# Kernel tuning notes

Measured on AMD Instinct MI355X. Metric: run time of the kernel, lower is better.

Reference implementation:

```python
import jax, jax.numpy as jnp
import numpy as np

SAMPLE_RATE = 44100
MAX_DURATION = 5.0
IR_LEN = int(SAMPLE_RATE * MAX_DURATION)   # 220500 taps (~5 s reverb tail)
AUDIO_LEN = SAMPLE_RATE * 60               # 60 s of mono audio


def setup_inputs() -> dict:
    key = jax.random.key(0)
    k1, k2 = jax.random.split(key)
    audio = jax.random.normal(k1, (1, AUDIO_LEN), dtype=jnp.float32)
    ir = jax.random.normal(k2, (IR_LEN,), dtype=jnp.float32)  # learned impulse response parameter
    return {"audio": audio, "ir": ir}


def _fft_correlate_valid(audio, ir):
    """Valid cross-correlation of (audio zero-padded by M-1) with ir.

    Matches torch: pad audio with M-1 trailing zeros, then conv1d (which is
    cross-correlation) in 'valid' mode -> output length N. Computed via FFT
    (O(N log N)) instead of direct O(N*M) convolution; identical math up to
    floating-point rounding.
    """
    B, N = audio.shape
    M = ir.shape[0]
    full = (N + M - 1) + M - 1          # full linear conv length of padded signal
    nfft = 1 << int(np.ceil(np.log2(full)))
    # trailing zero-pad covers both the explicit M-1 padding and FFT padding
    x = jnp.pad(audio, ((0, 0), (0, nfft - N)))
    k = jnp.pad(ir[::-1], (0, nfft - M))  # flip kernel: conv(x, flip(ir)) == correlate(x, ir)
    y = jnp.fft.irfft(jnp.fft.rfft(x, axis=-1) * jnp.fft.rfft(k), n=nfft, axis=-1)
    # valid cross-correlation region of the padded signal: indices [M-1, M-1+N)
    return jax.lax.dynamic_slice_in_dim(y, M - 1, N, axis=-1)


def reference(audio, ir):
    y = _fft_correlate_valid(audio, ir)       # [1, N]
    return y / jnp.max(jnp.abs(y))            # global max-abs normalization
```

## Files before the change

kernel.cpp:

```cpp
#include <hip/hip_runtime.h>
#include <hip/hip_fp16.h>


#define L_FFT (1 << 20)
#define GSTRIDE 273
#define PSCALE (1.0f / 1048576.0f)

__device__ __forceinline__ float2 h2f(__half2 h) { return __half22float2(h); }
__device__ __forceinline__ __half2 f2h(float2 v) { return __floats2half2_rn(v.x, v.y); }

__device__ __forceinline__ float2 cmul(float2 a, float2 b) {
    return make_float2(a.x * b.x - a.y * b.y, a.x * b.y + a.y * b.x);
}

__device__ __forceinline__ void rad4(float2 a, float2 b, float2 c, float2 d,
                                     float2& o0, float2& o1, float2& o2, float2& o3) {
    float2 apc = make_float2(a.x + c.x, a.y + c.y);
    float2 amc = make_float2(a.x - c.x, a.y - c.y);
    float2 bpd = make_float2(b.x + d.x, b.y + d.y);
    float2 bmd = make_float2(b.x - d.x, b.y - d.y);
    o0 = make_float2(apc.x + bpd.x, apc.y + bpd.y);
    o2 = make_float2(apc.x - bpd.x, apc.y - bpd.y);
    o1 = make_float2(amc.x + bmd.y, amc.y - bmd.x);
    o3 = make_float2(amc.x - bmd.y, amc.y + bmd.x);
}

__device__ __forceinline__ void dft16(float2 x[16]) {
    float2 tt[16];
    rad4(x[0], x[4], x[8],  x[12], tt[0],  tt[1],  tt[2],  tt[3]);
    rad4(x[1], x[5], x[9],  x[13], tt[4],  tt[5],  tt[6],  tt[7]);
    rad4(x[2], x[6], x[10], x[14], tt[8],  tt[9],  tt[10], tt[11]);
    rad4(x[3], x[7], x[11], x[15], tt[12], tt[13], tt[14], tt[15]);
    const float C1 = 0.92387953251128675613f, S1 = 0.38268343236508977173f;
    const float C2 = 0.70710678118654752440f;
    const float2 W1 = make_float2( C1, -S1);
    const float2 W2 = make_float2( C2, -C2);
    const float2 W3 = make_float2( S1, -C1);
    const float2 W6 = make_float2(-C2, -C2);
    const float2 W9 = make_float2(-C1,  S1);
    tt[5]  = cmul(tt[5],  W1);
    tt[6]  = cmul(tt[6],  W2);
    tt[7]  = cmul(tt[7],  W3);
    tt[9]  = cmul(tt[9],  W2);
    tt[10] = make_float2(tt[10].y, -tt[10].x);
    tt[11] = cmul(tt[11], W6);
    tt[13] = cmul(tt[13], W3);
    tt[14] = cmul(tt[14], W6);
    tt[15] = cmul(tt[15], W9);
    rad4(tt[0], tt[4], tt[8],  tt[12], x[0], x[4], x[8],  x[12]);
    rad4(tt[1], tt[5], tt[9],  tt[13], x[1], x[5], x[9],  x[13]);
    rad4(tt[2], tt[6], tt[10], tt[14], x[2], x[6], x[10], x[14]);
    rad4(tt[3], tt[7], tt[11], tt[15], x[3], x[7], x[11], x[15]);
}

__device__ __forceinline__ void fft256_core(float2 x[16], int i, int gi,
                                            float2* lds) {
    dft16(x);
    float sa, ca;
    __sincosf(-6.28318530717958647692f * (float)i * (1.0f / 256.0f), &sa, &ca);
    float2 w1 = make_float2(ca, sa);
    float2 w = w1;
#pragma unroll
    for (int k1 = 1; k1 < 16; ++k1) {
        x[k1] = cmul(x[k1], w);
        w = cmul(w, w1);
    }
    float2* base = lds + gi * GSTRIDE;
#pragma unroll
    for (int k1 = 0; k1 < 16; ++k1) base[i * 17 + k1] = x[k1];
    __syncthreads();
#pragma unroll
    for (int q1 = 0; q1 < 16; ++q1) x[q1] = base[q1 * 17 + i];
    dft16(x);
}

__device__ __forceinline__ void stage256_store(float2 x[16], __half2* db,
                                               int g, int i, int J, int log2J,
                                               float invLn) {
    int j = g & (J - 1);
    int np = g >> log2J;
    float base = -6.28318530717958647692f * (float)np * invLn;
    float sa, ca;
    __sincosf(base * (float)i, &sa, &ca);
    float2 w = make_float2(ca, sa);
    __sincosf(base * 16.0f, &sa, &ca);
    float2 w16 = make_float2(ca, sa);
    size_t ob = (size_t)256 * (g - j) + j;
#pragma unroll
    for (int k2 = 0; k2 < 16; ++k2) {
        db[ob + (size_t)(i + 16 * k2) * J] = f2h(cmul(x[k2], w));
        w = cmul(w, w16);
    }
}

__device__ __forceinline__ void store_j1_coalesced(float2 x[16], __half2* db,
                                                   int bx, int gi, int i, int tid,
                                                   float2* lds, float invL) {
    int g = bx * 16 + gi;
    float base = -6.28318530717958647692f * (float)g * invL;
    float sa, ca;
    __sincosf(base * (float)i, &sa, &ca);
    float2 w = make_float2(ca, sa);
    __sincosf(base * 16.0f, &sa, &ca);
    float2 w16 = make_float2(ca, sa);
    __syncthreads();
#pragma unroll
    for (int k2 = 0; k2 < 16; ++k2) {
        int e = 256 * gi + i + 16 * k2;
        lds[e + (e >> 8)] = cmul(x[k2], w);
        w = cmul(w, w16);
    }
    __syncthreads();
    __half2* dwin = db + (size_t)4096 * bx;
#pragma unroll
    for (int c = 0; c < 16; ++c) {
        int e2 = tid + 256 * c;
        dwin[e2] = f2h(lds[e2 + (e2 >> 8)]);
    }
}

__global__ void fwd1_pack(const float* __restrict__ audio,
                          const float* __restrict__ ir,
                          __half2* __restrict__ dst, int N, int M, int V) {
    __shared__ float2 lds[16 * GSTRIDE];
    int tid = threadIdx.x;
    int gi = tid & 15, i = tid >> 4;
    int bx = blockIdx.x, slot = blockIdx.y;
    int g = bx * 16 + gi;
    __half2* db = dst + (size_t)slot * L_FFT;

    float2 x[16];
#pragma unroll
    for (int q2 = 0; q2 < 16; ++q2) {
        int idx = g + (i + 16 * q2) * (L_FFT / 256);
        float2 v;
        if (slot == 0) {
            v = make_float2(audio[idx], audio[idx + V]);
        } else if (slot == 1) {
            float a2 = (idx + 2 * V < N) ? audio[idx + 2 * V] : 0.f;
            float a3 = (idx + 3 * V < N) ? audio[idx + 3 * V] : 0.f;
            v = make_float2(a2, a3);
        } else {
            v = make_float2((idx < M) ? ir[idx] : 0.f, 0.f);
        }
        x[q2] = v;
    }
    fft256_core(x, i, gi, lds);
    store_j1_coalesced(x, db, bx, gi, i, tid, lds, 1.0f / (float)L_FFT);
}

__global__ void stage256(const __half2* __restrict__ src, __half2* __restrict__ dst,
                         int J, int log2J, float invLn) {
    __shared__ float2 lds[16 * GSTRIDE];
    int tid = threadIdx.x;
    int gi = tid & 15, i = tid >> 4;
    int g = blockIdx.x * 16 + gi;
    size_t boff = (size_t)blockIdx.y * L_FFT;
    const __half2* sb = src + boff;
    __half2* db = dst + boff;
    float2 x[16];
#pragma unroll
    for (int q2 = 0; q2 < 16; ++q2)
        x[q2] = h2f(sb[g + (i + 16 * q2) * (L_FFT / 256)]);
    fft256_core(x, i, gi, lds);
    stage256_store(x, db, g, i, J, log2J, invLn);
}

__global__ void mid_spectral_inv1(const __half2* __restrict__ A,
                                  __half2* __restrict__ B) {
    __shared__ float2 lds[16 * GSTRIDE];
    int tid = threadIdx.x;
    int gi = tid & 15, i = tid >> 4;
    int bx = blockIdx.x;
    size_t boff = (size_t)blockIdx.y * L_FFT;
    int g = bx * 16 + gi;
    int gmid = g + (i << 12);

    const __half2* sa = A + boff;
    const __half2* sh = A + (size_t)2 * L_FFT;
    float2 x[16], h[16];
#pragma unroll
    for (int q = 0; q < 16; ++q) {
        x[q] = h2f(sa[gmid + (size_t)q * 65536]);
        h[q] = h2f(sh[gmid + (size_t)q * 65536]);
    }
    dft16(x);
    dft16(h);
#pragma unroll
    for (int r = 0; r < 16; ++r) {
        float2 Z = x[r], H = h[r];
        x[r] = make_float2((Z.x * H.x + Z.y * H.y) * PSCALE,
                           (Z.x * H.y - Z.y * H.x) * PSCALE);
    }
    fft256_core(x, i, gi, lds);
    store_j1_coalesced(x, B + boff, bx, gi, i, tid, lds, 1.0f / (float)L_FFT);
}

__global__ void inv3_max(const __half2* __restrict__ src,
                         float* __restrict__ partials, int N, int V) {
    int g = blockIdx.x * blockDim.x + threadIdx.x;
    int p = blockIdx.y;
    const __half2* sb = src + (size_t)p * L_FFT;
    float2 x[16];
#pragma unroll
    for (int q = 0; q < 16; ++q) x[q] = h2f(sb[g + q * 65536]);
    dft16(x);
    int lenO = (p == 1) ? (N - 3 * V) : V;
    float m = 0.f;
#pragma unroll
    for (int r = 0; r < 16; ++r) {
        int n = g + r * 65536;
        if (n < V)    m = fmaxf(m, fabsf(x[r].x));
        if (n < lenO) m = fmaxf(m, fabsf(x[r].y));
    }
    for (int o = 32; o > 0; o >>= 1) m = fmaxf(m, __shfl_xor(m, o));
    __shared__ float sm[4];
    int lane = threadIdx.x & 63, wv = threadIdx.x >> 6;
    if (lane == 0) sm[wv] = m;
    __syncthreads();
    if (threadIdx.x == 0)
        partials[blockIdx.y * gridDim.x + blockIdx.x] =
            fmaxf(fmaxf(sm[0], sm[1]), fmaxf(sm[2], sm[3]));
}

__global__ void norm_final(const __half2* __restrict__ src,
                           float* __restrict__ out,
                           const float* __restrict__ partials, int N, int V) {
    __shared__ float sm[4];
    int tid = threadIdx.x;
    int g = blockIdx.x * blockDim.x + tid;
    int p = blockIdx.y;
    const __half2* sb = src + (size_t)p * L_FFT;
    float2 x[16];
#pragma unroll
    for (int q = 0; q < 16; ++q) x[q] = h2f(sb[g + q * 65536]);

    float m = 0.f;
    for (int i = tid; i < 512; i += 256) m = fmaxf(m, partials[i]);
    for (int o = 32; o > 0; o >>= 1) m = fmaxf(m, __shfl_xor(m, o));
    int lane = tid & 63, wv = tid >> 6;
    if (lane == 0) sm[wv] = m;
    __syncthreads();
    float inv = 1.0f / fmaxf(fmaxf(sm[0], sm[1]), fmaxf(sm[2], sm[3]));

    dft16(x);
    int se = 2 * p, so = 2 * p + 1;
    int lenO = (p == 1) ? (N - 3 * V) : V;
#pragma unroll
    for (int r = 0; r < 16; ++r) {
        int n = g + r * 65536;
        if (n < V)    out[(size_t)se * V + n] = x[r].x * inv;
        if (n < lenO) out[(size_t)so * V + n] = -x[r].y * inv;
    }
}

extern "C" void kernel_launch(void* const* d_in, const int* in_sizes, int n_in,
                              void* d_out, int out_size, void* d_ws, size_t ws_size,
                              hipStream_t stream) {
    const float* audio = (const float*)d_in[0];
    const float* ir    = (const float*)d_in[1];
    float* out = (float*)d_out;

    const int N = in_sizes[0];
    const int M = in_sizes[1];
    const int V = L_FFT - M + 1;

    __half2* A = (__half2*)d_ws;
    __half2* B = A + (size_t)3 * L_FFT;
    float* partials = (float*)(B + (size_t)3 * L_FFT);

    const float invLn2 = 1.0f / 4096.0f;

    fwd1_pack<<<dim3(256, 3), 256, 0, stream>>>(audio, ir, B, N, M, V);
    stage256<<<dim3(256, 3), 256, 0, stream>>>(B, A, 256, 8, invLn2);
    mid_spectral_inv1<<<dim3(256, 2), 256, 0, stream>>>(A, B);
    stage256<<<dim3(256, 2), 256, 0, stream>>>(B, A, 256, 8, invLn2);
    inv3_max<<<dim3(256, 2), 256, 0, stream>>>(A, partials, N, V);
    norm_final<<<dim3(256, 2), 256, 0, stream>>>(A, out, partials, N, V);
}
```

Before: 117.6 us.

## Restructure FFT pipeline into 256x4096 decomposition with fused mid kernel

Replaces the three-pass 16x256x256 FFT chain with a two-pass 256x4096 decomposition. The second forward stage, the spectral multiply and the first inverse stage are fused into one block-local 4096-point FFT kernel, which cuts the launches from six to four and removes two full half-precision round trips through global memory. The first forward pass now writes strided (non-coalesced) output. The fused kernel uses two LDS buffers and more registers, which may lower occupancy.

```diff
diff --git a/kernel.cpp b/kernel.cpp
--- a/kernel.cpp
+++ b/kernel.cpp
@@ -74,49 +74,53 @@
     dft16(x);
 }
 
-__device__ __forceinline__ void stage256_store(float2 x[16], __half2* db,
-                                               int g, int i, int J, int log2J,
-                                               float invLn) {
-    int j = g & (J - 1);
-    int np = g >> log2J;
-    float base = -6.28318530717958647692f * (float)np * invLn;
-    float sa, ca;
-    __sincosf(base * (float)i, &sa, &ca);
-    float2 w = make_float2(ca, sa);
-    __sincosf(base * 16.0f, &sa, &ca);
-    float2 w16 = make_float2(ca, sa);
-    size_t ob = (size_t)256 * (g - j) + j;
-#pragma unroll
-    for (int k2 = 0; k2 < 16; ++k2) {
-        db[ob + (size_t)(i + 16 * k2) * J] = f2h(cmul(x[k2], w));
-        w = cmul(w, w16);
-    }
-}
-
-__device__ __forceinline__ void store_j1_coalesced(float2 x[16], __half2* db,
-                                                   int bx, int gi, int i, int tid,
-                                                   float2* lds, float invL) {
-    int g = bx * 16 + gi;
-    float base = -6.28318530717958647692f * (float)g * invL;
-    float sa, ca;
-    __sincosf(base * (float)i, &sa, &ca);
-    float2 w = make_float2(ca, sa);
-    __sincosf(base * 16.0f, &sa, &ca);
-    float2 w16 = make_float2(ca, sa);
-    __syncthreads();
-#pragma unroll
-    for (int k2 = 0; k2 < 16; ++k2) {
-        int e = 256 * gi + i + 16 * k2;
-        lds[e + (e >> 8)] = cmul(x[k2], w);
-        w = cmul(w, w16);
-    }
-    __syncthreads();
-    __half2* dwin = db + (size_t)4096 * bx;
-#pragma unroll
-    for (int c = 0; c < 16; ++c) {
-        int e2 = tid + 256 * c;
-        dwin[e2] = f2h(lds[e2 + (e2 >> 8)]);
-    }
+__device__ __forceinline__ void fft4096_block(float2 x[16], int tid, float2* lds) {
+    dft16(x);
+    float sa, ca;
+    __sincosf(-6.28318530717958647692f * (float)tid * (1.0f / 4096.0f), &sa, &ca);
+    float2 w1 = make_float2(ca, sa);
+    float2 w = w1;
+#pragma unroll
+    for (int a = 1; a < 16; ++a) { x[a] = cmul(x[a], w); w = cmul(w, w1); }
+#pragma unroll
+    for (int a = 0; a < 16; ++a) lds[a * GSTRIDE + tid] = x[a];
+    __syncthreads();
+    int an = tid & 15, i2 = tid >> 4;
+#pragma unroll
+    for (int q = 0; q < 16; ++q) x[q] = lds[an * GSTRIDE + i2 + 16 * q];
+    __syncthreads();
+    fft256_core(x, i2, an, lds);
+}
+
+__device__ __forceinline__ void fft4096_pair(float2 x[16], float2 h[16], int tid,
+                                             float2* LX, float2* LH) {
+    dft16(x);
+    dft16(h);
+    float sa, ca;
+    __sincosf(-6.28318530717958647692f * (float)tid * (1.0f / 4096.0f), &sa, &ca);
+    float2 w1 = make_float2(ca, sa);
+    float2 w = w1;
+#pragma unroll
+    for (int a = 1; a < 16; ++a) {
+        x[a] = cmul(x[a], w);
+        h[a] = cmul(h[a], w);
+        w = cmul(w, w1);
+    }
+#pragma unroll
+    for (int a = 0; a < 16; ++a) {
+        LX[a * GSTRIDE + tid] = x[a];
+        LH[a * GSTRIDE + tid] = h[a];
+    }
+    __syncthreads();
+    int an = tid & 15, i2 = tid >> 4;
+#pragma unroll
+    for (int q = 0; q < 16; ++q) {
+        x[q] = LX[an * GSTRIDE + i2 + 16 * q];
+        h[q] = LH[an * GSTRIDE + i2 + 16 * q];
+    }
+    __syncthreads();
+    fft256_core(x, i2, an, LX);
+    fft256_core(h, i2, an, LH);
 }
 
 __global__ void fwd1_pack(const float* __restrict__ audio,
@@ -146,109 +150,117 @@
         x[q2] = v;
     }
     fft256_core(x, i, gi, lds);
-    store_j1_coalesced(x, db, bx, gi, i, tid, lds, 1.0f / (float)L_FFT);
-}
-
-__global__ void stage256(const __half2* __restrict__ src, __half2* __restrict__ dst,
-                         int J, int log2J, float invLn) {
-    __shared__ float2 lds[16 * GSTRIDE];
-    int tid = threadIdx.x;
-    int gi = tid & 15, i = tid >> 4;
-    int g = blockIdx.x * 16 + gi;
-    size_t boff = (size_t)blockIdx.y * L_FFT;
-    const __half2* sb = src + boff;
-    __half2* db = dst + boff;
-    float2 x[16];
-#pragma unroll
-    for (int q2 = 0; q2 < 16; ++q2)
-        x[q2] = h2f(sb[g + (i + 16 * q2) * (L_FFT / 256)]);
-    fft256_core(x, i, gi, lds);
-    stage256_store(x, db, g, i, J, log2J, invLn);
-}
-
-__global__ void mid_spectral_inv1(const __half2* __restrict__ A,
-                                  __half2* __restrict__ B) {
-    __shared__ float2 lds[16 * GSTRIDE];
-    int tid = threadIdx.x;
-    int gi = tid & 15, i = tid >> 4;
-    int bx = blockIdx.x;
-    size_t boff = (size_t)blockIdx.y * L_FFT;
-    int g = bx * 16 + gi;
-    int gmid = g + (i << 12);
-
-    const __half2* sa = A + boff;
-    const __half2* sh = A + (size_t)2 * L_FFT;
+    float sa, ca;
+    float base = -6.28318530717958647692f * (float)g * (1.0f / (float)L_FFT);
+    __sincosf(base * (float)i, &sa, &ca);
+    float2 w = make_float2(ca, sa);
+    __sincosf(base * 16.0f, &sa, &ca);
+    float2 w16 = make_float2(ca, sa);
+#pragma unroll
+    for (int q = 0; q < 16; ++q) {
+        db[(size_t)4096 * (i + 16 * q) + g] = f2h(cmul(x[q], w));
+        w = cmul(w, w16);
+    }
+}
+
+__global__ __launch_bounds__(256, 2) void fused_mid(const __half2* __restrict__ Y1,
+                                                    __half2* __restrict__ Mp) {
+    __shared__ float2 LX[16 * GSTRIDE];
+    __shared__ float2 LH[16 * GSTRIDE];
+    int tid = threadIdx.x;
+    int b0 = blockIdx.x, p = blockIdx.y;
+    const __half2* xr = Y1 + (size_t)p * L_FFT + (size_t)4096 * b0;
+    const __half2* hr = Y1 + (size_t)2 * L_FFT + (size_t)4096 * b0;
     float2 x[16], h[16];
 #pragma unroll
-    for (int q = 0; q < 16; ++q) {
-        x[q] = h2f(sa[gmid + (size_t)q * 65536]);
-        h[q] = h2f(sh[gmid + (size_t)q * 65536]);
-    }
-    dft16(x);
-    dft16(h);
+    for (int w = 0; w < 16; ++w) {
+        x[w] = h2f(xr[tid + 256 * w]);
+        h[w] = h2f(hr[tid + 256 * w]);
+    }
+    fft4096_pair(x, h, tid, LX, LH);
 #pragma unroll
     for (int r = 0; r < 16; ++r) {
         float2 Z = x[r], H = h[r];
         x[r] = make_float2((Z.x * H.x + Z.y * H.y) * PSCALE,
                            (Z.x * H.y - Z.y * H.x) * PSCALE);
     }
+    fft4096_block(x, tid, LX);
+    float sa, ca;
+    float base = -6.28318530717958647692f * (float)b0 * (1.0f / (float)L_FFT);
+    __sincosf(base * (float)tid, &sa, &ca);
+    float2 w = make_float2(ca, sa);
+    __sincosf(base * 256.0f, &sa, &ca);
+    float2 ws = make_float2(ca, sa);
+    __half2* dst = Mp + (size_t)p * L_FFT + (size_t)4096 * b0;
+#pragma unroll
+    for (int r = 0; r < 16; ++r) {
+        dst[tid + 256 * r] = f2h(cmul(x[r], w));
+        w = cmul(w, ws);
+    }
+}
+
+__global__ void inv_max(const __half2* __restrict__ Mp,
+                        float* __restrict__ partials, int N, int V) {
+    __shared__ float2 lds[16 * GSTRIDE];
+    int tid = threadIdx.x;
+    int gi = tid & 15, i = tid >> 4;
+    int bx = blockIdx.x, p = blockIdx.y;
+    const __half2* sb = Mp + (size_t)p * L_FFT;
+    int na = 16 * bx + gi;
+    float2 x[16];
+#pragma unroll
+    for (int q = 0; q < 16; ++q)
+        x[q] = h2f(sb[(size_t)4096 * (i + 16 * q) + na]);
     fft256_core(x, i, gi, lds);
-    store_j1_coalesced(x, B + boff, bx, gi, i, tid, lds, 1.0f / (float)L_FFT);
-}
-
-__global__ void inv3_max(const __half2* __restrict__ src,
-                         float* __restrict__ partials, int N, int V) {
-    int g = blockIdx.x * blockDim.x + threadIdx.x;
-    int p = blockIdx.y;
-    const __half2* sb = src + (size_t)p * L_FFT;
-    float2 x[16];
-#pragma unroll
-    for (int q = 0; q < 16; ++q) x[q] = h2f(sb[g + q * 65536]);
-    dft16(x);
+    int nbase = na + 4096 * i;
     int lenO = (p == 1) ? (N - 3 * V) : V;
     float m = 0.f;
 #pragma unroll
     for (int r = 0; r < 16; ++r) {
-        int n = g + r * 65536;
+        int n = nbase + r * 65536;
         if (n < V)    m = fmaxf(m, fabsf(x[r].x));
         if (n < lenO) m = fmaxf(m, fabsf(x[r].y));
     }
     for (int o = 32; o > 0; o >>= 1) m = fmaxf(m, __shfl_xor(m, o));
     __shared__ float sm[4];
-    int lane = threadIdx.x & 63, wv = threadIdx.x >> 6;
+    int lane = tid & 63, wv = tid >> 6;
     if (lane == 0) sm[wv] = m;
     __syncthreads();
-    if (threadIdx.x == 0)
+    if (tid == 0)
         partials[blockIdx.y * gridDim.x + blockIdx.x] =
             fmaxf(fmaxf(sm[0], sm[1]), fmaxf(sm[2], sm[3]));
 }
 
-__global__ void norm_final(const __half2* __restrict__ src,
+__global__ void norm_write(const __half2* __restrict__ Mp,
                            float* __restrict__ out,
                            const float* __restrict__ partials, int N, int V) {
+    __shared__ float2 lds[16 * GSTRIDE];
     __shared__ float sm[4];
     int tid = threadIdx.x;
-    int g = blockIdx.x * blockDim.x + tid;
-    int p = blockIdx.y;
-    const __half2* sb = src + (size_t)p * L_FFT;
+    int gi = tid & 15, i = tid >> 4;
+    int bx = blockIdx.x, p = blockIdx.y;
+    const __half2* sb = Mp + (size_t)p * L_FFT;
+    int na = 16 * bx + gi;
     float2 x[16];
 #pragma unroll
-    for (int q = 0; q < 16; ++q) x[q] = h2f(sb[g + q * 65536]);
+    for (int q = 0; q < 16; ++q)
+        x[q] = h2f(sb[(size_t)4096 * (i + 16 * q) + na]);
 
     float m = 0.f;
-    for (int i = tid; i < 512; i += 256) m = fmaxf(m, partials[i]);
+    for (int t = tid; t < 512; t += 256) m = fmaxf(m, partials[t]);
     for (int o = 32; o > 0; o >>= 1) m = fmaxf(m, __shfl_xor(m, o));
     int lane = tid & 63, wv = tid >> 6;
     if (lane == 0) sm[wv] = m;
     __syncthreads();
     float inv = 1.0f / fmaxf(fmaxf(sm[0], sm[1]), fmaxf(sm[2], sm[3]));
 
-    dft16(x);
+    fft256_core(x, i, gi, lds);
+    int nbase = na + 4096 * i;
     int se = 2 * p, so = 2 * p + 1;
     int lenO = (p == 1) ? (N - 3 * V) : V;
 #pragma unroll
     for (int r = 0; r < 16; ++r) {
-        int n = g + r * 65536;
+        int n = nbase + r * 65536;
         if (n < V)    out[(size_t)se * V + n] = x[r].x * inv;
         if (n < lenO) out[(size_t)so * V + n] = -x[r].y * inv;
     }
@@ -269,12 +281,8 @@
     __half2* B = A + (size_t)3 * L_FFT;
     float* partials = (float*)(B + (size_t)3 * L_FFT);
 
-    const float invLn2 = 1.0f / 4096.0f;
-
     fwd1_pack<<<dim3(256, 3), 256, 0, stream>>>(audio, ir, B, N, M, V);
-    stage256<<<dim3(256, 3), 256, 0, stream>>>(B, A, 256, 8, invLn2);
-    mid_spectral_inv1<<<dim3(256, 2), 256, 0, stream>>>(A, B);
-    stage256<<<dim3(256, 2), 256, 0, stream>>>(B, A, 256, 8, invLn2);
-    inv3_max<<<dim3(256, 2), 256, 0, stream>>>(A, partials, N, V);
-    norm_final<<<dim3(256, 2), 256, 0, stream>>>(A, out, partials, N, V);
-}
+    fused_mid<<<dim3(256, 2), 256, 0, stream>>>(B, A);
+    inv_max<<<dim3(256, 2), 256, 0, stream>>>(A, partials, N, V);
+    norm_write<<<dim3(256, 2), 256, 0, stream>>>(A, out, partials, N, V);
+}
```

Measured after the change: 101.4 us. 13.8% less time.
